# Performance work log

Measured on AMD Instinct MI355X. Metric: run time of the kernel, lower is better.

## Reference

```python
import jax, jax.numpy as jnp
import numpy as np
import math

N_HEADS = 16

def setup_inputs() -> dict:
    key = jax.random.key(0)
    ks = jax.random.split(key, 6)
    bs, qlen, dim = 4, 2048, 1024
    s = 0.02  # param init scale
    return {
        "query": jax.random.normal(ks[0], (bs, qlen, dim), dtype=jnp.float32),
        "mask": jnp.ones((bs, qlen), dtype=jnp.int32),
        "Wq": jax.random.normal(ks[1], (dim, dim), dtype=jnp.float32) * s,
        "bq": jnp.zeros((dim,), dtype=jnp.float32),
        "Wk": jax.random.normal(ks[2], (dim, dim), dtype=jnp.float32) * s,
        "bk": jnp.zeros((dim,), dtype=jnp.float32),
        "Wv": jax.random.normal(ks[3], (dim, dim), dtype=jnp.float32) * s,
        "bv": jnp.zeros((dim,), dtype=jnp.float32),
        "Wo": jax.random.normal(ks[4], (dim, dim), dtype=jnp.float32) * s,
        "bo": jnp.zeros((dim,), dtype=jnp.float32),
    }


def reference(query, mask, Wq, bq, Wk, bk, Wv, bv, Wo, bo):
    bs, qlen, dim = query.shape
    h = N_HEADS
    dh = dim // h

    def shape(x):  # [b, s, dim] -> [b, h, s, dh]
        return x.reshape(bs, -1, h, dh).transpose(0, 2, 1, 3)

    q = shape(query @ Wq.T + bq) / math.sqrt(dh)
    k = shape(query @ Wk.T + bk)
    v = shape(query @ Wv.T + bv)

    scores = jnp.einsum("bhqd,bhkd->bhqk", q, k)  # [b, h, q, k]
    # 2-D mask -> (bs, 1, 1, klen); positions where mask==0 get -inf
    pad = (mask == 0)[:, None, None, :]
    scores = jnp.where(pad, -jnp.inf, scores)
    weights = jax.nn.softmax(scores.astype(jnp.float32), axis=-1).astype(scores.dtype)
    # dropout: eval mode (training=False) -> identity
    context = jnp.einsum("bhqk,bhkd->bhqd", weights, v)
    context = context.transpose(0, 2, 1, 3).reshape(bs, qlen, dim)
    out = context @ Wo.T + bo

    attn_scores = weights.sum(axis=1) / h          # [b, q, k]
    attn_scores_max = jnp.argmax(attn_scores, axis=-1)  # [b, q] int
    return out, attn_scores_max
```

## Files before the change

### kernel.cpp

```cpp
#include <hip/hip_runtime.h>
#include <math.h>
#include <type_traits>

#define BS   4
#define QLEN 2048
#define DIM  1024
#define NH   16
#define DH   64

#define GBM 64
#define GBN 64
#define GBK 32

template<bool F64>
__global__ __launch_bounds__(256)
void qkv_gemm(const float* __restrict__ X, const float* __restrict__ W,
              const float* __restrict__ bias, float* __restrict__ Out,
              float scale)
{
    using acc_t = typename std::conditional<F64, double, float>::type;
    __shared__ float xs[GBM][GBK + 1];
    __shared__ float wsm[GBN][GBK + 1];

    const int m0 = blockIdx.y * GBM;
    const int n0 = blockIdx.x * GBN;
    const int tid = threadIdx.x;
    const int tx = tid & 15, ty = tid >> 4;

    acc_t acc[4][4];
    #pragma unroll
    for (int i = 0; i < 4; ++i)
        #pragma unroll
        for (int j = 0; j < 4; ++j) acc[i][j] = (acc_t)0;

    for (int k0 = 0; k0 < DIM; k0 += GBK) {
        #pragma unroll
        for (int p = 0; p < 2; ++p) {
            int f4 = tid + p * 256;
            int row = f4 >> 3;
            int c4 = (f4 & 7) << 2;
            float4 xv = *(const float4*)&X[(size_t)(m0 + row) * DIM + k0 + c4];
            xs[row][c4] = xv.x; xs[row][c4+1] = xv.y; xs[row][c4+2] = xv.z; xs[row][c4+3] = xv.w;
            float4 wv = *(const float4*)&W[(size_t)(n0 + row) * DIM + k0 + c4];
            wsm[row][c4] = wv.x; wsm[row][c4+1] = wv.y; wsm[row][c4+2] = wv.z; wsm[row][c4+3] = wv.w;
        }
        __syncthreads();
        #pragma unroll
        for (int kk = 0; kk < GBK; ++kk) {
            float a[4], bb[4];
            #pragma unroll
            for (int i = 0; i < 4; ++i) a[i] = xs[ty * 4 + i][kk];
            #pragma unroll
            for (int j = 0; j < 4; ++j) bb[j] = wsm[tx * 4 + j][kk];
            if (F64) {
                #pragma unroll
                for (int i = 0; i < 4; ++i)
                    #pragma unroll
                    for (int j = 0; j < 4; ++j)
                        acc[i][j] = (acc_t)fma((double)a[i], (double)bb[j], (double)acc[i][j]);
            } else {
                #pragma unroll
                for (int i = 0; i < 4; ++i)
                    #pragma unroll
                    for (int j = 0; j < 4; ++j)
                        acc[i][j] = (acc_t)fmaf(a[i], bb[j], (float)acc[i][j]);
            }
        }
        __syncthreads();
    }

    #pragma unroll
    for (int i = 0; i < 4; ++i) {
        int row = m0 + ty * 4 + i;
        int b_ = row >> 11;
        int s_ = row & 2047;
        int col0 = n0 + tx * 4;
        int h_ = col0 >> 6, d_ = col0 & 63;
        float4 o;
        #pragma unroll
        for (int j = 0; j < 4; ++j) {
            acc_t v = (acc[i][j] + (acc_t)bias[col0 + j]) * (acc_t)scale;
            (&o.x)[j] = (float)v;
        }
        *(float4*)&Out[((size_t)((b_ * NH + h_) * QLEN + s_)) * DH + d_] = o;
    }
}

#define QT  16
#define QT2 32
#define KC  128
#define NCH (QLEN / KC)

__device__ __forceinline__ void pv_row(const float4& wr,
                                       const float4& v0, const float4& v1,
                                       const float4& v2, const float4& v3,
                                       float& c0, float& c1, float& c2, float& c3)
{
    c0 = fmaf(wr.x, v0.x, c0); c1 = fmaf(wr.x, v0.y, c1);
    c2 = fmaf(wr.x, v0.z, c2); c3 = fmaf(wr.x, v0.w, c3);
    c0 = fmaf(wr.y, v1.x, c0); c1 = fmaf(wr.y, v1.y, c1);
    c2 = fmaf(wr.y, v1.z, c2); c3 = fmaf(wr.y, v1.w, c3);
    c0 = fmaf(wr.z, v2.x, c0); c1 = fmaf(wr.z, v2.y, c1);
    c2 = fmaf(wr.z, v2.z, c2); c3 = fmaf(wr.z, v2.w, c3);
    c0 = fmaf(wr.w, v3.x, c0); c1 = fmaf(wr.w, v3.y, c1);
    c2 = fmaf(wr.w, v3.z, c2); c3 = fmaf(wr.w, v3.w, c3);
}

__global__ __launch_bounds__(512, 1)
void attn_kernel(const float* __restrict__ Qm, const float* __restrict__ Km,
                 const float* __restrict__ Vm, const int* __restrict__ mask,
                 float* __restrict__ ctx_out, float* __restrict__ MLbuf)
{
    __shared__ float qs[QT2][DH + 4];
    __shared__ __align__(16) float ks[KC][DH + 4];
    __shared__ float vs[KC][DH];
    __shared__ float wch[QT2][132];
    __shared__ int   msk[KC];
    __shared__ float m_lds[QT2];
    __shared__ float l_lds[QT2];
    __shared__ float scl[QT2];

    const int b   = blockIdx.y;
    const int q0  = blockIdx.x * QT2;
    const int tid = threadIdx.x;
    const int qp  = tid >> 5;
    const int kt2 = tid & 31;
    const int part = tid >> 7;
    const int sub  = tid & 127;
    const int pr   = (sub >> 4) << 2;
    const int pc4  = (sub & 15) << 2;

    #pragma unroll 1
    for (int h = 0; h < NH; ++h) {
        const float* Qh = Qm + (((size_t)b * NH + h) * QLEN + q0) * DH;
        const float* Kh = Km + ((size_t)b * NH + h) * QLEN * DH;
        const float* Vh = Vm + ((size_t)b * NH + h) * QLEN * DH;

        {
            int row = tid >> 4, c4 = (tid & 15) << 2;
            *(float4*)&qs[row][c4] = *(const float4*)&Qh[(size_t)row * DH + c4];
        }
        if (tid < QT2) { m_lds[tid] = -INFINITY; l_lds[tid] = 0.0f; }

        float cvA0 = 0.f, cvA1 = 0.f, cvA2 = 0.f, cvA3 = 0.f;
        float cvB0 = 0.f, cvB1 = 0.f, cvB2 = 0.f, cvB3 = 0.f;
        float cvC0 = 0.f, cvC1 = 0.f, cvC2 = 0.f, cvC3 = 0.f;
        float cvD0 = 0.f, cvD1 = 0.f, cvD2 = 0.f, cvD3 = 0.f;

        #pragma unroll 1
        for (int c = 0; c < NCH; ++c) {
            #pragma unroll
            for (int p = 0; p < 4; ++p) {
                int f4 = tid + p * 512;
                int row = f4 >> 4, c4 = (f4 & 15) << 2;
                *(float4*)&ks[row][c4] = *(const float4*)&Kh[(size_t)(c * KC + row) * DH + c4];
                *(float4*)&vs[row][c4] = *(const float4*)&Vh[(size_t)(c * KC + row) * DH + c4];
            }
            if (tid < KC) msk[tid] = mask[b * QLEN + c * KC + tid];
            __syncthreads();

            float s0[4], s1[4];
            #pragma unroll
            for (int jj = 0; jj < 4; ++jj) { s0[jj] = 0.f; s1[jj] = 0.f; }
            #pragma unroll
            for (int d0 = 0; d0 < DH; d0 += 4) {
                float4 qv0 = *(const float4*)&qs[qp][d0];
                float4 qv1 = *(const float4*)&qs[qp + 16][d0];
                #pragma unroll
                for (int jj = 0; jj < 4; ++jj) {
                    float4 kv = *(const float4*)&ks[kt2 + 32 * jj][d0];
                    s0[jj] = fmaf(qv0.x, kv.x, s0[jj]);
                    s0[jj] = fmaf(qv0.y, kv.y, s0[jj]);
                    s0[jj] = fmaf(qv0.z, kv.z, s0[jj]);
                    s0[jj] = fmaf(qv0.w, kv.w, s0[jj]);
                    s1[jj] = fmaf(qv1.x, kv.x, s1[jj]);
                    s1[jj] = fmaf(qv1.y, kv.y, s1[jj]);
                    s1[jj] = fmaf(qv1.z, kv.z, s1[jj]);
                    s1[jj] = fmaf(qv1.w, kv.w, s1[jj]);
                }
            }
            float mm0 = -INFINITY, mm1 = -INFINITY;
            #pragma unroll
            for (int jj = 0; jj < 4; ++jj) {
                s0[jj] = msk[kt2 + 32 * jj] ? s0[jj] : -INFINITY;
                s1[jj] = msk[kt2 + 32 * jj] ? s1[jj] : -INFINITY;
                mm0 = fmaxf(mm0, s0[jj]);
                mm1 = fmaxf(mm1, s1[jj]);
            }
            #pragma unroll
            for (int off = 1; off < 32; off <<= 1) {
                mm0 = fmaxf(mm0, __shfl_xor(mm0, off, 64));
                mm1 = fmaxf(mm1, __shfl_xor(mm1, off, 64));
            }
            float mold0 = m_lds[qp], mold1 = m_lds[qp + 16];
            float mnew0 = fmaxf(mold0, mm0), mnew1 = fmaxf(mold1, mm1);
            float sc0 = (mnew0 > -INFINITY) ? __expf(mold0 - mnew0) : 0.0f;
            float sc1 = (mnew1 > -INFINITY) ? __expf(mold1 - mnew1) : 0.0f;
            float ls0 = 0.f, ls1 = 0.f;
            #pragma unroll
            for (int jj = 0; jj < 4; ++jj) {
                float w0 = (s0[jj] > -INFINITY) ? __expf(s0[jj] - mnew0) : 0.0f;
                float w1 = (s1[jj] > -INFINITY) ? __expf(s1[jj] - mnew1) : 0.0f;
                wch[qp][kt2 + 32 * jj]      = w0;
                wch[qp + 16][kt2 + 32 * jj] = w1;
                ls0 += w0;
                ls1 += w1;
            }
            #pragma unroll
            for (int off = 1; off < 32; off <<= 1) {
                ls0 += __shfl_xor(ls0, off, 64);
                ls1 += __shfl_xor(ls1, off, 64);
            }
            if (kt2 == 0) {
                l_lds[qp]      = l_lds[qp]      * sc0 + ls0;
                l_lds[qp + 16] = l_lds[qp + 16] * sc1 + ls1;
                m_lds[qp]      = mnew0;
                m_lds[qp + 16] = mnew1;
                scl[qp]        = sc0;
                scl[qp + 16]   = sc1;
            }
            __syncthreads();

            {
                float sA = scl[pr], sB = scl[pr + 1], sC = scl[pr + 2], sD = scl[pr + 3];
                cvA0 *= sA; cvA1 *= sA; cvA2 *= sA; cvA3 *= sA;
                cvB0 *= sB; cvB1 *= sB; cvB2 *= sB; cvB3 *= sB;
                cvC0 *= sC; cvC1 *= sC; cvC2 *= sC; cvC3 *= sC;
                cvD0 *= sD; cvD1 *= sD; cvD2 *= sD; cvD3 *= sD;
                const int kbase = part * 32;
                #pragma unroll 2
                for (int kk = 0; kk < 32; kk += 4) {
                    int k0 = kbase + kk;
                    float4 wA = *(const float4*)&wch[pr    ][k0];
                    float4 wB = *(const float4*)&wch[pr + 1][k0];
                    float4 wC = *(const float4*)&wch[pr + 2][k0];
                    float4 wD = *(const float4*)&wch[pr + 3][k0];
                    float4 v0 = *(const float4*)&vs[k0    ][pc4];
                    float4 v1 = *(const float4*)&vs[k0 + 1][pc4];
                    float4 v2 = *(const float4*)&vs[k0 + 2][pc4];
                    float4 v3 = *(const float4*)&vs[k0 + 3][pc4];
                    pv_row(wA, v0, v1, v2, v3, cvA0, cvA1, cvA2, cvA3);
                    pv_row(wB, v0, v1, v2, v3, cvB0, cvB1, cvB2, cvB3);
                    pv_row(wC, v0, v1, v2, v3, cvC0, cvC1, cvC2, cvC3);
                    pv_row(wD, v0, v1, v2, v3, cvD0, cvD1, cvD2, cvD3);
                }
            }
            __syncthreads();
        }

        float4* red4 = (float4*)&ks[0][0];
        if (part != 0) {
            int base = sub * 12 + (part - 1) * 4;
            red4[base + 0] = make_float4(cvA0, cvA1, cvA2, cvA3);
            red4[base + 1] = make_float4(cvB0, cvB1, cvB2, cvB3);
            red4[base + 2] = make_float4(cvC0, cvC1, cvC2, cvC3);
            red4[base + 3] = make_float4(cvD0, cvD1, cvD2, cvD3);
        }
        __syncthreads();
        if (part == 0) {
            #pragma unroll
            for (int p = 0; p < 3; ++p) {
                int base = sub * 12 + p * 4;
                float4 rA = red4[base + 0], rB = red4[base + 1];
                float4 rC = red4[base + 2], rD = red4[base + 3];
                cvA0 += rA.x; cvA1 += rA.y; cvA2 += rA.z; cvA3 += rA.w;
                cvB0 += rB.x; cvB1 += rB.y; cvB2 += rB.z; cvB3 += rB.w;
                cvC0 += rC.x; cvC1 += rC.y; cvC2 += rC.z; cvC3 += rC.w;
                cvD0 += rD.x; cvD1 += rD.y; cvD2 += rD.z; cvD3 += rD.w;
            }
            float LA = l_lds[pr], LB = l_lds[pr + 1], LC = l_lds[pr + 2], LD = l_lds[pr + 3];
            float* base = ctx_out + ((size_t)(b * QLEN + q0)) * DIM + h * DH + pc4;
            *(float4*)&base[(size_t)(pr    ) * DIM] = make_float4(cvA0 / LA, cvA1 / LA, cvA2 / LA, cvA3 / LA);
            *(float4*)&base[(size_t)(pr + 1) * DIM] = make_float4(cvB0 / LB, cvB1 / LB, cvB2 / LB, cvB3 / LB);
            *(float4*)&base[(size_t)(pr + 2) * DIM] = make_float4(cvC0 / LC, cvC1 / LC, cvC2 / LC, cvC3 / LC);
            *(float4*)&base[(size_t)(pr + 3) * DIM] = make_float4(cvD0 / LD, cvD1 / LD, cvD2 / LD, cvD3 / LD);
        }
        if (tid < QT2) {
            float* mlp = MLbuf + (((size_t)(b * QLEN + q0 + tid)) * NH + h) * 2;
            mlp[0] = m_lds[tid];
            mlp[1] = l_lds[tid];
        }
        __syncthreads();
    }
}

__global__ __launch_bounds__(512, 4)
void hsum_argmax_kernel(const float* __restrict__ Qm, const float* __restrict__ Km,
                        const int* __restrict__ mask, const float* __restrict__ MLbuf,
                        float* __restrict__ idx_out)
{
    __shared__ float qs[QT][DH + 4];
    __shared__ float ks[KC][DH + 4];
    __shared__ float Mh[NH][QT];
    __shared__ float Lh[NH][QT];
    __shared__ int   msk[KC];
    __shared__ float rv[512];
    __shared__ int   ri[512];

    const int b   = blockIdx.y;
    const int q0  = blockIdx.x * QT;
    const int tid = threadIdx.x;
    const int q   = tid >> 5;
    const int kt  = tid & 31;

    if (tid < NH * QT) {
        int h = tid >> 4, qq = tid & 15;
        const float* mlp = MLbuf + (((size_t)(b * QLEN + q0 + qq)) * NH + h) * 2;
        Mh[h][qq] = mlp[0];
        Lh[h][qq] = mlp[1];
    }

    float bv = -1.0f; int bk = 0;
    #pragma unroll 1
    for (int c = 0; c < NCH; ++c) {
        float h0 = 0.f, h1 = 0.f, h2 = 0.f, h3 = 0.f;
        #pragma unroll 1
        for (int h = 0; h < NH; ++h) {
            __syncthreads();
            const float* Kh = Km + ((size_t)b * NH + h) * QLEN * DH;
            #pragma unroll
            for (int p = 0; p < 4; ++p) {
                int f4 = tid + p * 512;
                int row = f4 >> 4, c4 = (f4 & 15) << 2;
                *(float4*)&ks[row][c4] = *(const float4*)&Kh[(size_t)(c * KC + row) * DH + c4];
            }
            if (tid < 256) {
                int row = tid >> 4, c4 = (tid & 15) << 2;
                const float* Qh = Qm + (((size_t)b * NH + h) * QLEN + q0) * DH;
                *(float4*)&qs[row][c4] = *(const float4*)&Qh[(size_t)row * DH + c4];
            }
            if (h == 0 && tid < KC) msk[tid] = mask[b * QLEN + c * KC + tid];
            __syncthreads();

            float sacc[4] = {0.f, 0.f, 0.f, 0.f};
            #pragma unroll
            for (int d0 = 0; d0 < DH; d0 += 4) {
                float4 qv = *(const float4*)&qs[q][d0];
                #pragma unroll
                for (int jj = 0; jj < 4; ++jj) {
                    float4 kv = *(const float4*)&ks[kt + 32 * jj][d0];
                    sacc[jj] = fmaf(qv.x, kv.x, sacc[jj]);
                    sacc[jj] = fmaf(qv.y, kv.y, sacc[jj]);
                    sacc[jj] = fmaf(qv.z, kv.z, sacc[jj]);
                    sacc[jj] = fmaf(qv.w, kv.w, sacc[jj]);
                }
            }
            const float Mv = Mh[h][q], Lv = Lh[h][q];
            float s0 = msk[kt]      ? sacc[0] : -INFINITY;
            float s1 = msk[kt + 32] ? sacc[1] : -INFINITY;
            float s2 = msk[kt + 64] ? sacc[2] : -INFINITY;
            float s3 = msk[kt + 96] ? sacc[3] : -INFINITY;
            h0 += expf(s0 - Mv) / Lv;
            h1 += expf(s1 - Mv) / Lv;
            h2 += expf(s2 - Mv) / Lv;
            h3 += expf(s3 - Mv) / Lv;
        }
        int kbase = c * KC + kt;
        if (h0 > bv) { bv = h0; bk = kbase;      }
        if (h1 > bv) { bv = h1; bk = kbase + 32; }
        if (h2 > bv) { bv = h2; bk = kbase + 64; }
        if (h3 > bv) { bv = h3; bk = kbase + 96; }
    }

    rv[tid] = bv;
    ri[tid] = bk;
    __syncthreads();
    if (kt == 0) {
        float BV = -1.0f; int BKi = 1 << 30;
        for (int i = 0; i < 32; ++i) {
            float v = rv[q * 32 + i];
            int  kk = ri[q * 32 + i];
            if (v > BV || (v == BV && kk < BKi)) { BV = v; BKi = kk; }
        }
        idx_out[b * QLEN + q0 + q] = (float)BKi;
    }
}

#define OPROWS 16

__global__ __launch_bounds__(512, 2)
void outproj_kernel(float* __restrict__ IO, const float* __restrict__ Wo,
                    const float* __restrict__ bo)
{
    __shared__ float ctxs[OPROWS][DIM];
    __shared__ float wos[64][132];

    const int m0 = blockIdx.x * OPROWS;
    const int tid = threadIdx.x;
    const int q = tid >> 5, kt = tid & 31;

    #pragma unroll
    for (int p = 0; p < 8; ++p) {
        int f4 = tid + p * 512;
        int row = f4 >> 8;
        int c4 = (f4 & 255) << 2;
        *(float4*)&ctxs[row][c4] = *(const float4*)&IO[(size_t)(m0 + row) * DIM + c4];
    }
    __syncthreads();

    #pragma unroll 1
    for (int oc = 0; oc < DIM / 64; ++oc) {
        float a0 = 0.f, a1 = 0.f;
        #pragma unroll 1
        for (int d0 = 0; d0 < DIM; d0 += 128) {
            #pragma unroll
            for (int p = 0; p < 4; ++p) {
                int f4 = tid + p * 512;
                int row = f4 >> 5, c4 = (f4 & 31) << 2;
                *(float4*)&wos[row][c4] =
                    *(const float4*)&Wo[(size_t)(oc * 64 + row) * DIM + d0 + c4];
            }
            __syncthreads();
            #pragma unroll 4
            for (int dd = 0; dd < 128; dd += 4) {
                float4 cv = *(const float4*)&ctxs[q][d0 + dd];
                float4 w0 = *(const float4*)&wos[kt][dd];
                float4 w1 = *(const float4*)&wos[32 + kt][dd];
                a0 = fmaf(cv.x, w0.x, a0);
                a0 = fmaf(cv.y, w0.y, a0);
                a0 = fmaf(cv.z, w0.z, a0);
                a0 = fmaf(cv.w, w0.w, a0);
                a1 = fmaf(cv.x, w1.x, a1);
                a1 = fmaf(cv.y, w1.y, a1);
                a1 = fmaf(cv.z, w1.z, a1);
                a1 = fmaf(cv.w, w1.w, a1);
            }
            __syncthreads();
        }
        int o0 = oc * 64 + kt;
        IO[(size_t)(m0 + q) * DIM + o0]      = a0 + bo[o0];
        IO[(size_t)(m0 + q) * DIM + o0 + 32] = a1 + bo[o0 + 32];
    }
}

extern "C" void kernel_launch(void* const* d_in, const int* in_sizes, int n_in,
                              void* d_out, int out_size, void* d_ws, size_t ws_size,
                              hipStream_t stream)
{
    (void)in_sizes; (void)n_in; (void)out_size; (void)ws_size;
    const float* query = (const float*)d_in[0];
    const int*   mask  = (const int*)  d_in[1];
    const float* Wq = (const float*)d_in[2];
    const float* bq = (const float*)d_in[3];
    const float* Wk = (const float*)d_in[4];
    const float* bk = (const float*)d_in[5];
    const float* Wv = (const float*)d_in[6];
    const float* bv = (const float*)d_in[7];
    const float* Wo = (const float*)d_in[8];
    const float* bo = (const float*)d_in[9];

    float* out = (float*)d_out;
    const size_t NTOK = (size_t)BS * QLEN;
    const size_t QKV  = NTOK * DIM;
    float* Qw = (float*)d_ws;
    float* Kw = Qw + QKV;
    float* Vw = Kw + QKV;
    float* ML = Vw + QKV;

    dim3 gemm_grid(DIM / GBN, (BS * QLEN) / GBM);
    qkv_gemm<false><<<gemm_grid, dim3(256), 0, stream>>>(query, Wq, bq, Qw, 0.125f);
    qkv_gemm<false><<<gemm_grid, dim3(256), 0, stream>>>(query, Wk, bk, Kw, 1.0f);
    qkv_gemm<false><<<gemm_grid, dim3(256), 0, stream>>>(query, Wv, bv, Vw, 1.0f);

    float* ctx = out;
    float* idx = out + NTOK * DIM;
    attn_kernel<<<dim3(QLEN / QT2, BS), dim3(512), 0, stream>>>(Qw, Kw, Vw, mask, ctx, ML);
    hsum_argmax_kernel<<<dim3(QLEN / QT, BS), dim3(512), 0, stream>>>(Qw, Kw, mask, ML, idx);
    outproj_kernel<<<dim3(NTOK / OPROWS), dim3(512), 0, stream>>>(out, Wo, bo);
}
```

Measured before the change: 3.988 ms.

## Vectorize QKV GEMM LDS reads and double query rows per hsum-argmax block

```diff
diff --git a/kernel.cpp b/kernel.cpp
--- a/kernel.cpp
+++ b/kernel.cpp
@@ -1,6 +1,5 @@
 #include <hip/hip_runtime.h>
 #include <math.h>
-#include <type_traits>
 
 #define BS   4
 #define QLEN 2048
@@ -11,27 +10,26 @@
 #define GBM 64
 #define GBN 64
 #define GBK 32
-
-template<bool F64>
+#define GST (GBK + 4)
+
 __global__ __launch_bounds__(256)
 void qkv_gemm(const float* __restrict__ X, const float* __restrict__ W,
               const float* __restrict__ bias, float* __restrict__ Out,
               float scale)
 {
-    using acc_t = typename std::conditional<F64, double, float>::type;
-    __shared__ float xs[GBM][GBK + 1];
-    __shared__ float wsm[GBN][GBK + 1];
+    __shared__ float xs[GBM][GST];
+    __shared__ float wsm[GBN][GST];
 
     const int m0 = blockIdx.y * GBM;
     const int n0 = blockIdx.x * GBN;
     const int tid = threadIdx.x;
     const int tx = tid & 15, ty = tid >> 4;
 
-    acc_t acc[4][4];
+    float acc[4][4];
     #pragma unroll
     for (int i = 0; i < 4; ++i)
         #pragma unroll
-        for (int j = 0; j < 4; ++j) acc[i][j] = (acc_t)0;
+        for (int j = 0; j < 4; ++j) acc[i][j] = 0.f;
 
     for (int k0 = 0; k0 < DIM; k0 += GBK) {
         #pragma unroll
@@ -39,54 +37,45 @@
             int f4 = tid + p * 256;
             int row = f4 >> 3;
             int c4 = (f4 & 7) << 2;
-            float4 xv = *(const float4*)&X[(size_t)(m0 + row) * DIM + k0 + c4];
-            xs[row][c4] = xv.x; xs[row][c4+1] = xv.y; xs[row][c4+2] = xv.z; xs[row][c4+3] = xv.w;
-            float4 wv = *(const float4*)&W[(size_t)(n0 + row) * DIM + k0 + c4];
-            wsm[row][c4] = wv.x; wsm[row][c4+1] = wv.y; wsm[row][c4+2] = wv.z; wsm[row][c4+3] = wv.w;
+            *(float4*)&xs[row][c4]  = *(const float4*)&X[(size_t)(m0 + row) * DIM + k0 + c4];
+            *(float4*)&wsm[row][c4] = *(const float4*)&W[(size_t)(n0 + row) * DIM + k0 + c4];
         }
         __syncthreads();
         #pragma unroll
-        for (int kk = 0; kk < GBK; ++kk) {
-            float a[4], bb[4];
-            #pragma unroll
-            for (int i = 0; i < 4; ++i) a[i] = xs[ty * 4 + i][kk];
-            #pragma unroll
-            for (int j = 0; j < 4; ++j) bb[j] = wsm[tx * 4 + j][kk];
-            if (F64) {
+        for (int kk = 0; kk < GBK; kk += 4) {
+            float4 a4[4], b4[4];
+            #pragma unroll
+            for (int i = 0; i < 4; ++i) a4[i] = *(const float4*)&xs[ty + 16 * i][kk];
+            #pragma unroll
+            for (int j = 0; j < 4; ++j) b4[j] = *(const float4*)&wsm[tx + 16 * j][kk];
+            #pragma unroll
+            for (int i = 0; i < 4; ++i)
                 #pragma unroll
-                for (int i = 0; i < 4; ++i)
-                    #pragma unroll
-                    for (int j = 0; j < 4; ++j)
-                        acc[i][j] = (acc_t)fma((double)a[i], (double)bb[j], (double)acc[i][j]);
-            } else {
-                #pragma unroll
-                for (int i = 0; i < 4; ++i)
-                    #pragma unroll
-                    for (int j = 0; j < 4; ++j)
-                        acc[i][j] = (acc_t)fmaf(a[i], bb[j], (float)acc[i][j]);
-            }
+                for (int j = 0; j < 4; ++j) {
+                    acc[i][j] = fmaf(a4[i].x, b4[j].x, acc[i][j]);
+                    acc[i][j] = fmaf(a4[i].y, b4[j].y, acc[i][j]);
+                    acc[i][j] = fmaf(a4[i].z, b4[j].z, acc[i][j]);
+                    acc[i][j] = fmaf(a4[i].w, b4[j].w, acc[i][j]);
+                }
         }
         __syncthreads();
     }
 
     #pragma unroll
     for (int i = 0; i < 4; ++i) {
-        int row = m0 + ty * 4 + i;
+        int row = m0 + ty + 16 * i;
         int b_ = row >> 11;
         int s_ = row & 2047;
-        int col0 = n0 + tx * 4;
-        int h_ = col0 >> 6, d_ = col0 & 63;
-        float4 o;
         #pragma unroll
         for (int j = 0; j < 4; ++j) {
-            acc_t v = (acc[i][j] + (acc_t)bias[col0 + j]) * (acc_t)scale;
-            (&o.x)[j] = (float)v;
-        }
-        *(float4*)&Out[((size_t)((b_ * NH + h_) * QLEN + s_)) * DH + d_] = o;
-    }
-}
-
-#define QT  16
+            int col = n0 + tx + 16 * j;
+            int h_ = col >> 6, d_ = col & 63;
+            float v = (acc[i][j] + bias[col]) * scale;
+            Out[((size_t)((b_ * NH + h_) * QLEN + s_)) * DH + d_] = v;
+        }
+    }
+}
+
 #define QT2 32
 #define KC  128
 #define NCH (QLEN / KC)
@@ -250,7 +239,7 @@
 
         float4* red4 = (float4*)&ks[0][0];
         if (part != 0) {
-            int base = sub * 12 + (part - 1) * 4;
+            int base = sub * 13 + (part - 1) * 4;
             red4[base + 0] = make_float4(cvA0, cvA1, cvA2, cvA3);
             red4[base + 1] = make_float4(cvB0, cvB1, cvB2, cvB3);
             red4[base + 2] = make_float4(cvC0, cvC1, cvC2, cvC3);
@@ -260,7 +249,7 @@
         if (part == 0) {
             #pragma unroll
             for (int p = 0; p < 3; ++p) {
-                int base = sub * 12 + p * 4;
+                int base = sub * 13 + p * 4;
                 float4 rA = red4[base + 0], rB = red4[base + 1];
                 float4 rC = red4[base + 2], rD = red4[base + 3];
                 cvA0 += rA.x; cvA1 += rA.y; cvA2 += rA.z; cvA3 += rA.w;
@@ -289,31 +278,32 @@
                         const int* __restrict__ mask, const float* __restrict__ MLbuf,
                         float* __restrict__ idx_out)
 {
-    __shared__ float qs[QT][DH + 4];
+    __shared__ float qs[QT2][DH + 4];
     __shared__ float ks[KC][DH + 4];
-    __shared__ float Mh[NH][QT];
-    __shared__ float Lh[NH][QT];
+    __shared__ float Mh[NH][QT2];
+    __shared__ float Lh[NH][QT2];
     __shared__ int   msk[KC];
-    __shared__ float rv[512];
-    __shared__ int   ri[512];
+    __shared__ float rv[2][16][32];
+    __shared__ int   ri[2][16][32];
 
     const int b   = blockIdx.y;
-    const int q0  = blockIdx.x * QT;
+    const int q0  = blockIdx.x * QT2;
     const int tid = threadIdx.x;
-    const int q   = tid >> 5;
-    const int kt  = tid & 31;
-
-    if (tid < NH * QT) {
-        int h = tid >> 4, qq = tid & 15;
-        const float* mlp = MLbuf + (((size_t)(b * QLEN + q0 + qq)) * NH + h) * 2;
-        Mh[h][qq] = mlp[0];
-        Lh[h][qq] = mlp[1];
-    }
-
-    float bv = -1.0f; int bk = 0;
+    const int qp  = tid >> 5;
+    const int kt2 = tid & 31;
+
+    {
+        int h = tid >> 5, rr = tid & 31;
+        const float* mlp = MLbuf + (((size_t)(b * QLEN + q0 + rr)) * NH + h) * 2;
+        Mh[h][rr] = mlp[0];
+        Lh[h][rr] = mlp[1];
+    }
+
+    float bv0 = -1.0f, bv1 = -1.0f; int bk0 = 0, bk1 = 0;
     #pragma unroll 1
     for (int c = 0; c < NCH; ++c) {
-        float h0 = 0.f, h1 = 0.f, h2 = 0.f, h3 = 0.f;
+        float a00 = 0.f, a01 = 0.f, a02 = 0.f, a03 = 0.f;
+        float a10 = 0.f, a11 = 0.f, a12 = 0.f, a13 = 0.f;
         #pragma unroll 1
         for (int h = 0; h < NH; ++h) {
             __syncthreads();
@@ -324,55 +314,69 @@
                 int row = f4 >> 4, c4 = (f4 & 15) << 2;
                 *(float4*)&ks[row][c4] = *(const float4*)&Kh[(size_t)(c * KC + row) * DH + c4];
             }
-            if (tid < 256) {
+            {
+                const float* Qh = Qm + (((size_t)b * NH + h) * QLEN + q0) * DH;
                 int row = tid >> 4, c4 = (tid & 15) << 2;
-                const float* Qh = Qm + (((size_t)b * NH + h) * QLEN + q0) * DH;
                 *(float4*)&qs[row][c4] = *(const float4*)&Qh[(size_t)row * DH + c4];
             }
             if (h == 0 && tid < KC) msk[tid] = mask[b * QLEN + c * KC + tid];
             __syncthreads();
 
-            float sacc[4] = {0.f, 0.f, 0.f, 0.f};
-            #pragma unroll
+            float s0[4], s1[4];
+            #pragma unroll
+            for (int jj = 0; jj < 4; ++jj) { s0[jj] = 0.f; s1[jj] = 0.f; }
+            #pragma unroll 4
             for (int d0 = 0; d0 < DH; d0 += 4) {
-                float4 qv = *(const float4*)&qs[q][d0];
+                float4 qv0 = *(const float4*)&qs[qp][d0];
+                float4 qv1 = *(const float4*)&qs[qp + 16][d0];
                 #pragma unroll
                 for (int jj = 0; jj < 4; ++jj) {
-                    float4 kv = *(const float4*)&ks[kt + 32 * jj][d0];
-                    sacc[jj] = fmaf(qv.x, kv.x, sacc[jj]);
-                    sacc[jj] = fmaf(qv.y, kv.y, sacc[jj]);
-                    sacc[jj] = fmaf(qv.z, kv.z, sacc[jj]);
-                    sacc[jj] = fmaf(qv.w, kv.w, sacc[jj]);
+                    float4 kv = *(const float4*)&ks[kt2 + 32 * jj][d0];
+                    s0[jj] = fmaf(qv0.x, kv.x, s0[jj]);
+                    s0[jj] = fmaf(qv0.y, kv.y, s0[jj]);
+                    s0[jj] = fmaf(qv0.z, kv.z, s0[jj]);
+                    s0[jj] = fmaf(qv0.w, kv.w, s0[jj]);
+                    s1[jj] = fmaf(qv1.x, kv.x, s1[jj]);
+                    s1[jj] = fmaf(qv1.y, kv.y, s1[jj]);
+                    s1[jj] = fmaf(qv1.z, kv.z, s1[jj]);
+                    s1[jj] = fmaf(qv1.w, kv.w, s1[jj]);
                 }
             }
-            const float Mv = Mh[h][q], Lv = Lh[h][q];
-            float s0 = msk[kt]      ? sacc[0] : -INFINITY;
-            float s1 = msk[kt + 32] ? sacc[1] : -INFINITY;
-            float s2 = msk[kt + 64] ? sacc[2] : -INFINITY;
-            float s3 = msk[kt + 96] ? sacc[3] : -INFINITY;
-            h0 += expf(s0 - Mv) / Lv;
-            h1 += expf(s1 - Mv) / Lv;
-            h2 += expf(s2 - Mv) / Lv;
-            h3 += expf(s3 - Mv) / Lv;
-        }
-        int kbase = c * KC + kt;
-        if (h0 > bv) { bv = h0; bk = kbase;      }
-        if (h1 > bv) { bv = h1; bk = kbase + 32; }
-        if (h2 > bv) { bv = h2; bk = kbase + 64; }
-        if (h3 > bv) { bv = h3; bk = kbase + 96; }
-    }
-
-    rv[tid] = bv;
-    ri[tid] = bk;
+            const float Mv0 = Mh[h][qp],      Lv0 = Lh[h][qp];
+            const float Mv1 = Mh[h][qp + 16], Lv1 = Lh[h][qp + 16];
+            int mk0 = msk[kt2], mk1 = msk[kt2 + 32], mk2 = msk[kt2 + 64], mk3 = msk[kt2 + 96];
+            a00 += mk0 ? expf(s0[0] - Mv0) / Lv0 : 0.f;
+            a01 += mk1 ? expf(s0[1] - Mv0) / Lv0 : 0.f;
+            a02 += mk2 ? expf(s0[2] - Mv0) / Lv0 : 0.f;
+            a03 += mk3 ? expf(s0[3] - Mv0) / Lv0 : 0.f;
+            a10 += mk0 ? expf(s1[0] - Mv1) / Lv1 : 0.f;
+            a11 += mk1 ? expf(s1[1] - Mv1) / Lv1 : 0.f;
+            a12 += mk2 ? expf(s1[2] - Mv1) / Lv1 : 0.f;
+            a13 += mk3 ? expf(s1[3] - Mv1) / Lv1 : 0.f;
+        }
+        int kbase = c * KC + kt2;
+        if (a00 > bv0) { bv0 = a00; bk0 = kbase;      }
+        if (a01 > bv0) { bv0 = a01; bk0 = kbase + 32; }
+        if (a02 > bv0) { bv0 = a02; bk0 = kbase + 64; }
+        if (a03 > bv0) { bv0 = a03; bk0 = kbase + 96; }
+        if (a10 > bv1) { bv1 = a10; bk1 = kbase;      }
+        if (a11 > bv1) { bv1 = a11; bk1 = kbase + 32; }
+        if (a12 > bv1) { bv1 = a12; bk1 = kbase + 64; }
+        if (a13 > bv1) { bv1 = a13; bk1 = kbase + 96; }
+    }
+
+    rv[0][qp][kt2] = bv0; ri[0][qp][kt2] = bk0;
+    rv[1][qp][kt2] = bv1; ri[1][qp][kt2] = bk1;
     __syncthreads();
-    if (kt == 0) {
+    if (tid < QT2) {
+        int half = tid >> 4, qq = tid & 15;
         float BV = -1.0f; int BKi = 1 << 30;
         for (int i = 0; i < 32; ++i) {
-            float v = rv[q * 32 + i];
-            int  kk = ri[q * 32 + i];
+            float v = rv[half][qq][i];
+            int  kk = ri[half][qq][i];
             if (v > BV || (v == BV && kk < BKi)) { BV = v; BKi = kk; }
         }
-        idx_out[b * QLEN + q0 + q] = (float)BKi;
+        idx_out[b * QLEN + q0 + half * 16 + qq] = (float)BKi;
     }
 }
 
@@ -458,13 +462,13 @@
     float* ML = Vw + QKV;
 
     dim3 gemm_grid(DIM / GBN, (BS * QLEN) / GBM);
-    qkv_gemm<false><<<gemm_grid, dim3(256), 0, stream>>>(query, Wq, bq, Qw, 0.125f);
-    qkv_gemm<false><<<gemm_grid, dim3(256), 0, stream>>>(query, Wk, bk, Kw, 1.0f);
-    qkv_gemm<false><<<gemm_grid, dim3(256), 0, stream>>>(query, Wv, bv, Vw, 1.0f);
+    qkv_gemm<<<gemm_grid, dim3(256), 0, stream>>>(query, Wq, bq, Qw, 0.125f);
+    qkv_gemm<<<gemm_grid, dim3(256), 0, stream>>>(query, Wk, bk, Kw, 1.0f);
+    qkv_gemm<<<gemm_grid, dim3(256), 0, stream>>>(query, Wv, bv, Vw, 1.0f);
 
     float* ctx = out;
     float* idx = out + NTOK * DIM;
     attn_kernel<<<dim3(QLEN / QT2, BS), dim3(512), 0, stream>>>(Qw, Kw, Vw, mask, ctx, ML);
-    hsum_argmax_kernel<<<dim3(QLEN / QT, BS), dim3(512), 0, stream>>>(Qw, Kw, mask, ML, idx);
+    hsum_argmax_kernel<<<dim3(QLEN / QT2, BS), dim3(512), 0, stream>>>(Qw, Kw, mask, ML, idx);
     outproj_kernel<<<dim3(NTOK / OPROWS), dim3(512), 0, stream>>>(out, Wo, bo);
 }
```

New measurement: 3.913 ms. No clear change (-1.9%).
